# Kernel tuning notes

Measured on AMD Instinct MI355X. Metric: run time of the kernel, lower is better.

## Reference

```python
import jax, jax.numpy as jnp
import numpy as np

DIM = 1024
HEADS = 16
HEAD_DIM = 64
CHUNK = 128
B = 2
S = 2048  # 2 * N * CHUNK with N = 8


def rotate_half(x):
    # interleaved pair rotation: (x1, x2) -> (-x2, x1)
    x1 = x[..., 0::2]
    x2 = x[..., 1::2]
    return jnp.stack((-x2, x1), axis=-1).reshape(x.shape)


def rms_norm(x, w, eps=1e-6):
    v = jnp.mean(jnp.square(x.astype(jnp.float32)), axis=-1, keepdims=True)
    return (x * jax.lax.rsqrt(v + eps)).astype(x.dtype) * w


def build_chunk_mask(seq_len, chunk_size):
    # Replicates ChunkAttnProcessor training mask (right_mask).
    c = jnp.arange(seq_len) // chunk_size
    ci = c[None, :]   # key-chunk index (columns) -- matches torch's unsqueeze(0)
    cj = c[:, None]   # query-chunk index (rows)  -- matches torch's unsqueeze(1)
    N = seq_len // (2 * chunk_size)  # num_cache_blocks
    max_lookback = 5
    rel_j = cj - N
    mask_self = ci == cj
    mask_cache = (rel_j >= 0) & (ci < N) & (ci < rel_j) & (ci >= rel_j - max_lookback)
    return mask_self | mask_cache  # [S, S] bool, row = query, col = key


def setup_inputs() -> dict:
    key = jax.random.key(0)
    ks = jax.random.split(key, 10)
    x = jax.random.normal(ks[0], (B, S, DIM), jnp.float32)
    mask = jnp.ones((B, S), jnp.bool_)
    # rotary frequency table, interleaved pairs: [S, HEAD_DIM]
    pos = jnp.arange(S, dtype=jnp.float32)
    inv = 1.0 / (10000.0 ** (jnp.arange(0, HEAD_DIM, 2, dtype=jnp.float32) / HEAD_DIM))
    freqs = jnp.repeat(pos[:, None] * inv[None, :], 2, axis=-1)
    inner = HEADS * HEAD_DIM
    sc = 0.02
    Wq = jax.random.normal(ks[1], (inner, DIM), jnp.float32) * sc
    bq = jax.random.normal(ks[2], (inner,), jnp.float32) * sc
    Wk = jax.random.normal(ks[3], (inner, DIM), jnp.float32) * sc
    bk = jax.random.normal(ks[4], (inner,), jnp.float32) * sc
    Wv = jax.random.normal(ks[5], (inner, DIM), jnp.float32) * sc
    bv = jax.random.normal(ks[6], (inner,), jnp.float32) * sc
    Wo = jax.random.normal(ks[7], (DIM, inner), jnp.float32) * sc
    bo = jax.random.normal(ks[8], (DIM,), jnp.float32) * sc
    qw = jnp.ones((HEAD_DIM,), jnp.float32)
    kw = jnp.ones((HEAD_DIM,), jnp.float32)
    return {"x": x, "mask": mask, "freqs": freqs, "Wq": Wq, "bq": bq,
            "Wk": Wk, "bk": bk, "Wv": Wv, "bv": bv, "Wo": Wo, "bo": bo,
            "qw": qw, "kw": kw}


def reference(x, mask, freqs, Wq, bq, Wk, bk, Wv, bv, Wo, bo, qw, kw):
    b, n, _ = x.shape
    # QKV projections (torch Linear: x @ W.T + b)
    q = jnp.einsum('bnd,ed->bne', x, Wq) + bq
    k = jnp.einsum('bnd,ed->bne', x, Wk) + bk
    v = jnp.einsum('bnd,ed->bne', x, Wv) + bv
    q = q.reshape(b, n, HEADS, HEAD_DIM).transpose(0, 2, 1, 3)  # [b,h,n,d]
    k = k.reshape(b, n, HEADS, HEAD_DIM).transpose(0, 2, 1, 3)
    v = v.reshape(b, n, HEADS, HEAD_DIM).transpose(0, 2, 1, 3)
    # qk rms-norm over head_dim
    q = rms_norm(q, qw)
    k = rms_norm(k, kw)
    # rotary embedding (xpos_scale = None -> scale 1.0)
    cos = jnp.cos(freqs)
    sin = jnp.sin(freqs)
    q = q * cos + rotate_half(q) * sin
    k = k * cos + rotate_half(k) * sin
    # block-local + cache-lookback mask (training path), combined with pad mask
    block_mask = build_chunk_mask(n, CHUNK)                                  # [S,S]
    pad = (mask[:, None, :] & mask[:, :, None]) | jnp.eye(n, dtype=bool)[None]
    amask = (block_mask[None] & pad)[:, None]                                # [b,1,S,S]
    # masked SDPA
    scale = 1.0 / np.sqrt(HEAD_DIM)
    logits = jnp.einsum('bhqd,bhkd->bhqk', q, k) * scale
    logits = jnp.where(amask, logits, -jnp.inf)
    attn = jax.nn.softmax(logits, axis=-1)
    o = jnp.einsum('bhqk,bhkd->bhqd', attn, v)
    o = o.transpose(0, 2, 1, 3).reshape(b, n, HEADS * HEAD_DIM)
    o = jnp.einsum('bne,de->bnd', o, Wo) + bo
    o = jnp.where(mask[..., None], o, 0.0)
    return o
```

## Files before the change

### kernel.cpp

```cpp
#include <hip/hip_runtime.h>
#include <stdint.h>

typedef unsigned short u16;
typedef __bf16 bf16x8 __attribute__((ext_vector_type(8)));
typedef float f32x4 __attribute__((ext_vector_type(4)));
typedef u16 u16x8 __attribute__((ext_vector_type(8)));

#define DIMD 1024
#define SLEN 2048
#define NHEAD 16
#define HD 64

static __device__ __forceinline__ float b2f(u16 u){ union{float f;uint32_t i;}x; x.i=((uint32_t)u)<<16; return x.f; }
static __device__ __forceinline__ u16 f2b(float f){ union{float f;uint32_t i;}x; x.f=f; uint32_t r=x.i+0x7FFFu+((x.i>>16)&1u); return (u16)(r>>16); }
static __device__ __forceinline__ u16 f2b_fast(float f){ __bf16 h=(__bf16)f; return __builtin_bit_cast(u16,h); }

static __device__ __forceinline__ void gl_lds16(const u16* g, u16* l){
  __builtin_amdgcn_global_load_lds((__attribute__((address_space(1))) void*)g,
                                   (__attribute__((address_space(3))) void*)l, 16, 0, 0);
}
static __device__ __forceinline__ f32x4 mfma16(bf16x8 a, bf16x8 b, f32x4 c){
  return __builtin_amdgcn_mfma_f32_16x16x32_bf16(a, b, c, 0, 0, 0);
}

__global__ __launch_bounds__(256) void k_convert(const float* __restrict__ x,
    const float* __restrict__ wq, const float* __restrict__ wk,
    const float* __restrict__ wv, const float* __restrict__ wo,
    u16* __restrict__ ws)
{
  const int y = blockIdx.y;
  const float* src; u16* dst; int n;
  if (y==0){ src=x;  dst=ws;           n=1<<22; }
  else if (y==1){ src=wq; dst=ws+(4u<<20); n=1<<20; }
  else if (y==2){ src=wk; dst=ws+(5u<<20); n=1<<20; }
  else if (y==3){ src=wv; dst=ws+(6u<<20); n=1<<20; }
  else          { src=wo; dst=ws+(7u<<20); n=1<<20; }
  const int idx = (blockIdx.x*256 + threadIdx.x)*8;
  if (idx >= n) return;
  const float4* s4 = (const float4*)(src+idx);
  float4 a = s4[0], b = s4[1];
  u16x8 r;
  r[0]=f2b(a.x); r[1]=f2b(a.y); r[2]=f2b(a.z); r[3]=f2b(a.w);
  r[4]=f2b(b.x); r[5]=f2b(b.y); r[6]=f2b(b.z); r[7]=f2b(b.w);
  *(u16x8*)(dst+idx) = r;
}

__global__ __launch_bounds__(256,2) void k_gemm_qkv(const u16* __restrict__ A,
    const u16* __restrict__ wq, const u16* __restrict__ wk, const u16* __restrict__ wv,
    const float* __restrict__ bq, const float* __restrict__ bk, const float* __restrict__ bv,
    u16* __restrict__ qo, u16* __restrict__ ko, u16* __restrict__ vo)
{
  __shared__ u16 Al[128*32];
  __shared__ u16 Bl[128*32];
  const int tid = threadIdx.x, lane = tid&63, w = tid>>6;
  const int L15 = lane&15, g = lane>>4;
  const int mb = blockIdx.x;
  const int yy = blockIdx.y;
  const int t = yy>>3, nb = yy&7;
  const u16* Bm = (t==0)?wq:((t==1)?wk:wv);
  const float* bias = (t==0)?bq:((t==1)?bk:bv);
  u16* dst = (t==0)?qo:((t==1)?ko:vo);
  const int wm=(w&1)*64, wn=(w>>1)*64;
  f32x4 acc[4][4];
  #pragma unroll
  for(int i=0;i<4;++i){
    #pragma unroll
    for(int j=0;j<4;++j) acc[i][j]=0;
  }
  const u16* Ab = A  + (size_t)mb*128*DIMD;
  const u16* Bb = Bm + (size_t)nb*128*DIMD;
  const int srow = lane>>2, scol = (lane&3)*8;
  for (int kt=0; kt<32; ++kt){
    const int kk = kt*32;
    #pragma unroll
    for (int c2=0;c2<2;++c2){
      const int c = w*2+c2;
      gl_lds16(Ab + (c*16+srow)*DIMD + kk + scol, Al + c*512);
      gl_lds16(Bb + (c*16+srow)*DIMD + kk + scol, Bl + c*512);
    }
    __syncthreads();
    bf16x8 af[4], bf[4];
    #pragma unroll
    for (int mt=0;mt<4;++mt) af[mt]=*(const bf16x8*)(Al + (wm+mt*16+L15)*32 + g*8);
    #pragma unroll
    for (int nt=0;nt<4;++nt) bf[nt]=*(const bf16x8*)(Bl + (wn+nt*16+L15)*32 + g*8);
    #pragma unroll
    for (int mt=0;mt<4;++mt){
      #pragma unroll
      for (int nt=0;nt<4;++nt)
        acc[mt][nt]=mfma16(af[mt], bf[nt], acc[mt][nt]);
    }
    __syncthreads();
  }
  #pragma unroll
  for (int nt=0;nt<4;++nt){
    const int c = nb*128 + wn + nt*16 + L15;
    const float bv_ = bias[c];
    const int h = c>>6, d = c&63;
    #pragma unroll
    for (int mt=0;mt<4;++mt){
      #pragma unroll
      for (int r=0;r<4;++r){
        const int rowM = mb*128 + wm + mt*16 + g*4 + r;
        const int b_ = rowM>>11, s = rowM&(SLEN-1);
        dst[((size_t)((b_*NHEAD+h)*SLEN+s))*HD + d] = f2b(acc[mt][nt][r]+bv_);
      }
    }
  }
}

__global__ __launch_bounds__(256,2) void k_gemm_out(const u16* __restrict__ A,
    const u16* __restrict__ Bm, const float* __restrict__ bias, float* __restrict__ out)
{
  __shared__ u16 Al[128*32];
  __shared__ u16 Bl[128*32];
  const int tid = threadIdx.x, lane = tid&63, w = tid>>6;
  const int L15 = lane&15, g = lane>>4;
  const int mb = blockIdx.x;
  const int nb = blockIdx.y;
  const int wm=(w&1)*64, wn=(w>>1)*64;
  f32x4 acc[4][4];
  #pragma unroll
  for(int i=0;i<4;++i){
    #pragma unroll
    for(int j=0;j<4;++j) acc[i][j]=0;
  }
  const u16* Ab = A  + (size_t)mb*128*DIMD;
  const u16* Bb = Bm + (size_t)nb*128*DIMD;
  const int srow = lane>>2, scol = (lane&3)*8;
  for (int kt=0; kt<32; ++kt){
    const int kk = kt*32;
    #pragma unroll
    for (int c2=0;c2<2;++c2){
      const int c = w*2+c2;
      gl_lds16(Ab + (c*16+srow)*DIMD + kk + scol, Al + c*512);
      gl_lds16(Bb + (c*16+srow)*DIMD + kk + scol, Bl + c*512);
    }
    __syncthreads();
    bf16x8 af[4], bf[4];
    #pragma unroll
    for (int mt=0;mt<4;++mt) af[mt]=*(const bf16x8*)(Al + (wm+mt*16+L15)*32 + g*8);
    #pragma unroll
    for (int nt=0;nt<4;++nt) bf[nt]=*(const bf16x8*)(Bl + (wn+nt*16+L15)*32 + g*8);
    #pragma unroll
    for (int mt=0;mt<4;++mt){
      #pragma unroll
      for (int nt=0;nt<4;++nt)
        acc[mt][nt]=mfma16(af[mt], bf[nt], acc[mt][nt]);
    }
    __syncthreads();
  }
  #pragma unroll
  for (int nt=0;nt<4;++nt){
    const int c = nb*128 + wn + nt*16 + L15;
    const float bv_ = bias[c];
    #pragma unroll
    for (int mt=0;mt<4;++mt){
      #pragma unroll
      for (int r=0;r<4;++r){
        const int rowM = mb*128 + wm + mt*16 + g*4 + r;
        out[(size_t)rowM*DIMD + c] = acc[mt][nt][r]+bv_;
      }
    }
  }
}

__global__ __launch_bounds__(256) void k_rope(u16* __restrict__ qb, u16* __restrict__ kb,
    const float* __restrict__ freqs, const float* __restrict__ qw, const float* __restrict__ kw)
{
  const int tid=threadIdx.x, lane=tid&63, w=tid>>6;
  const int rid = blockIdx.x*4 + w;
  u16* buf; const float* wt; float scale;
  if (blockIdx.y==0){ buf=qb; wt=qw; scale=0.125f; } else { buf=kb; wt=kw; scale=1.0f; }
  const int s = rid & (SLEN-1);
  const size_t off = (size_t)rid*HD + lane;
  float v = b2f(buf[off]);
  float ss = v*v;
  #pragma unroll
  for (int m=32;m;m>>=1) ss += __shfl_xor(ss, m);
  float xn = v * rsqrtf(ss*(1.0f/HD) + 1e-6f) * wt[lane];
  float fr = freqs[s*HD + lane];
  float cs = __cosf(fr), sn = __sinf(fr);
  float pa = __shfl_xor(xn, 1);
  float rot = (lane&1) ? pa : -pa;
  buf[off] = f2b((xn*cs + rot*sn)*scale);
}

__global__ __launch_bounds__(256,2) void k_attn(const u16* __restrict__ qb, const u16* __restrict__ kb,
    const u16* __restrict__ vb, u16* __restrict__ ob)
{
  __shared__ u16 VT[64*128];
  __shared__ u16 Kl[128*64];
  __shared__ u16 Pl[4*32*128];
  const int tid=threadIdx.x, lane=tid&63, w=tid>>6;
  const int L15=lane&15, g=lane>>4;
  const int bid=blockIdx.x;
  const int qc=bid&15, h=(bid>>4)&15, b_=bid>>8;
  const size_t bh=(size_t)(b_*NHEAD+h);
  const u16* qp = qb + (bh*SLEN + qc*128)*HD;

  bf16x8 qf[2][2];
  #pragma unroll
  for (int mt=0;mt<2;++mt){
    #pragma unroll
    for (int ks=0;ks<2;++ks)
      qf[mt][ks]=*(const bf16x8*)(qp + (w*32+mt*16+L15)*HD + ks*32 + g*8);
  }

  f32x4 accO[2][4];
  float ps[2][4];
  #pragma unroll
  for (int mt=0;mt<2;++mt){
    #pragma unroll
    for(int nt=0;nt<4;++nt) accO[mt][nt]=0;
    #pragma unroll
    for(int r=0;r<4;++r) ps[mt][r]=0.f;
  }

  int kcs[6]; int nk=0; kcs[nk++]=qc;
  if (qc>=9){
    int lo=qc-13; if(lo<0)lo=0;
    const int hi=qc-9;
    for(int kc=lo;kc<=hi;++kc) kcs[nk++]=kc;
  }
  u16* Pw = Pl + w*32*128;

  for (int it=0; it<nk; ++it){
    const int kc=kcs[it];
    const u16* kp = kb + (bh*SLEN + kc*128)*HD;
    const u16* vp = vb + (bh*SLEN + kc*128)*HD;
    #pragma unroll
    for (int i=0;i<4;++i){
      const int idx = i*256 + tid;
      const int row = idx>>3, k8 = idx&7;
      u16x8 kv = *(const u16x8*)(kp + row*HD + k8*8);
      *(u16x8*)(Kl + row*HD + 8*(k8 ^ (row&7))) = kv;
    }
    #pragma unroll
    for (int p=0;p<2;++p){
      const int k0 = p*64 + (tid&31)*2;
      const int dc = (tid>>5)*8;
      u16x8 v0 = *(const u16x8*)(vp + k0*HD + dc);
      u16x8 v1 = *(const u16x8*)(vp + (k0+1)*HD + dc);
      #pragma unroll
      for (int j=0;j<8;++j){
        const int d = dc+j;
        const int kx = k0 ^ ((d&7)<<3);
        *(uint32_t*)(VT + d*128 + kx) = (uint32_t)v0[j] | ((uint32_t)v1[j]<<16);
      }
    }
    __syncthreads();
    #pragma unroll
    for (int mt=0;mt<2;++mt){
      f32x4 sfr[8];
      #pragma unroll
      for (int nt=0;nt<8;++nt){
        const int row = nt*16+L15;
        const u16* kr = Kl + row*HD;
        bf16x8 kf0 = *(const bf16x8*)(kr + 8*((g  ) ^ (row&7)));
        bf16x8 kf1 = *(const bf16x8*)(kr + 8*((g+4) ^ (row&7)));
        f32x4 cc=0;
        cc=mfma16(qf[mt][0],kf0,cc);
        cc=mfma16(qf[mt][1],kf1,cc);
        sfr[nt]=cc;
      }
      #pragma unroll
      for (int nt=0;nt<8;++nt){
        const int col=nt*16+L15;
        #pragma unroll
        for (int r=0;r<4;++r){
          float pv=__expf(sfr[nt][r]);
          ps[mt][r]+=pv;
          const int row=mt*16+g*4+r;
          Pw[row*128 + (col ^ ((row&15)<<3))]=f2b_fast(pv);
        }
      }
    }
    #pragma unroll
    for (int ks=0;ks<4;++ks){
      bf16x8 pf[2], vf[4];
      #pragma unroll
      for (int mt=0;mt<2;++mt){
        const int row=mt*16+L15;
        pf[mt]=*(const bf16x8*)(Pw + row*128 + ((ks*32+g*8) ^ ((row&15)<<3)));
      }
      #pragma unroll
      for (int nt=0;nt<4;++nt){
        const int n=nt*16+L15;
        vf[nt]=*(const bf16x8*)(VT + n*128 + ((ks*32+g*8) ^ ((n&7)<<3)));
      }
      #pragma unroll
      for (int mt=0;mt<2;++mt){
        #pragma unroll
        for (int nt=0;nt<4;++nt)
          accO[mt][nt]=mfma16(pf[mt],vf[nt],accO[mt][nt]);
      }
    }
    __syncthreads();
  }

  #pragma unroll
  for (int mt=0;mt<2;++mt){
    #pragma unroll
    for (int r=0;r<4;++r){
      float l=ps[mt][r];
      #pragma unroll
      for (int sh=1; sh<16; sh<<=1) l+=__shfl_xor(l,sh);
      const float inv=1.0f/l;
      const int srow=qc*128 + w*32 + mt*16 + g*4 + r;
      #pragma unroll
      for (int nt=0;nt<4;++nt){
        const size_t di=((size_t)(b_*SLEN+srow))*DIMD + h*HD + nt*16 + L15;
        ob[di]=f2b_fast(accO[mt][nt][r]*inv);
      }
    }
  }
}

extern "C" void kernel_launch(void* const* d_in, const int* in_sizes, int n_in,
                              void* d_out, int out_size, void* d_ws, size_t ws_size,
                              hipStream_t stream)
{
  (void)in_sizes; (void)n_in; (void)out_size; (void)ws_size;
  const float* x     = (const float*)d_in[0];
  const float* freqs = (const float*)d_in[2];
  const float* Wq    = (const float*)d_in[3];
  const float* bq    = (const float*)d_in[4];
  const float* Wk    = (const float*)d_in[5];
  const float* bk    = (const float*)d_in[6];
  const float* Wv    = (const float*)d_in[7];
  const float* bv    = (const float*)d_in[8];
  const float* Wo    = (const float*)d_in[9];
  const float* bo    = (const float*)d_in[10];
  const float* qw    = (const float*)d_in[11];
  const float* kw    = (const float*)d_in[12];

  u16* ws  = (u16*)d_ws;
  u16* xb  = ws;
  u16* wqb = ws + (4u<<20);
  u16* wkb = ws + (5u<<20);
  u16* wvb = ws + (6u<<20);
  u16* wob = ws + (7u<<20);
  u16* q   = ws + (8u<<20);
  u16* k   = ws + (12u<<20);
  u16* v   = ws + (16u<<20);
  u16* o   = ws + (20u<<20);

  k_convert<<<dim3(2048,5),256,0,stream>>>(x,Wq,Wk,Wv,Wo,ws);
  k_gemm_qkv<<<dim3(32,24),256,0,stream>>>(xb,wqb,wkb,wvb,bq,bk,bv,q,k,v);
  k_rope<<<dim3(16384,2),256,0,stream>>>(q,k,freqs,qw,kw);
  k_attn<<<512,256,0,stream>>>(q,k,v,o);
  k_gemm_out<<<dim3(32,8),256,0,stream>>>(o,wob,bo,(float*)d_out);
}
```

Before: 198.6 us.

## Fuse QK RMS-norm and rotary into QKV GEMM epilogue; reorder attention chunks

The separate rope kernel is removed. RMS-norm, rotary embedding and the q scaling now run in the QKV GEMM epilogue, using cross-lane shuffles over the 16-lane groups that each hold one head's 64 columns. This drops a kernel launch and a full read-modify-write pass over q and k. Separately, the attention block-to-chunk mapping is reversed for batch 1, likely to spread the uneven per-chunk work across the grid. The epilogue gets heavier, with more shuffles and transcendental calls per GEMM tile, which may raise register pressure.

```diff
diff --git a/kernel.cpp b/kernel.cpp
--- a/kernel.cpp
+++ b/kernel.cpp
@@ -48,6 +48,7 @@
 __global__ __launch_bounds__(256,2) void k_gemm_qkv(const u16* __restrict__ A,
     const u16* __restrict__ wq, const u16* __restrict__ wk, const u16* __restrict__ wv,
     const float* __restrict__ bq, const float* __restrict__ bk, const float* __restrict__ bv,
+    const float* __restrict__ freqs, const float* __restrict__ qw, const float* __restrict__ kw,
     u16* __restrict__ qo, u16* __restrict__ ko, u16* __restrict__ vo)
 {
   __shared__ u16 Al[128*32];
@@ -92,18 +93,54 @@
     }
     __syncthreads();
   }
-  #pragma unroll
-  for (int nt=0;nt<4;++nt){
-    const int c = nb*128 + wn + nt*16 + L15;
-    const float bv_ = bias[c];
-    const int h = c>>6, d = c&63;
+  float bias_v[4];
+  #pragma unroll
+  for (int nt=0;nt<4;++nt) bias_v[nt] = bias[nb*128 + wn + nt*16 + L15];
+
+  if (t < 2){
+    const float* wt = (t==0)? qw : kw;
+    const float scale = (t==0)? 0.125f : 1.0f;
+    const int h = (nb*128 + wn) >> 6;
+    float wt_v[4];
+    #pragma unroll
+    for (int nt=0;nt<4;++nt) wt_v[nt] = wt[nt*16 + L15];
     #pragma unroll
     for (int mt=0;mt<4;++mt){
       #pragma unroll
       for (int r=0;r<4;++r){
+        float val[4]; float ss=0.f;
+        #pragma unroll
+        for (int nt=0;nt<4;++nt){ val[nt]=acc[mt][nt][r]+bias_v[nt]; ss+=val[nt]*val[nt]; }
+        #pragma unroll
+        for (int sh=1; sh<16; sh<<=1) ss += __shfl_xor(ss, sh);
+        const float rin = rsqrtf(ss*(1.0f/HD) + 1e-6f);
         const int rowM = mb*128 + wm + mt*16 + g*4 + r;
-        const int b_ = rowM>>11, s = rowM&(SLEN-1);
-        dst[((size_t)((b_*NHEAD+h)*SLEN+s))*HD + d] = f2b(acc[mt][nt][r]+bv_);
+        const int b2 = rowM>>11, s = rowM&(SLEN-1);
+        const size_t rb = ((size_t)((b2*NHEAD+h)*SLEN+s))*HD;
+        #pragma unroll
+        for (int nt=0;nt<4;++nt){
+          const int d = nt*16 + L15;
+          float xn = val[nt]*rin*wt_v[nt];
+          float fr = freqs[s*HD + d];
+          float pa = __shfl_xor(xn, 1);
+          float rot = (L15&1) ? pa : -pa;
+          dst[rb + d] = f2b((xn*__cosf(fr) + rot*__sinf(fr))*scale);
+        }
+      }
+    }
+  } else {
+    #pragma unroll
+    for (int nt=0;nt<4;++nt){
+      const int c = nb*128 + wn + nt*16 + L15;
+      const int h = c>>6, d = c&63;
+      #pragma unroll
+      for (int mt=0;mt<4;++mt){
+        #pragma unroll
+        for (int r=0;r<4;++r){
+          const int rowM = mb*128 + wm + mt*16 + g*4 + r;
+          const int b2 = rowM>>11, s = rowM&(SLEN-1);
+          dst[((size_t)((b2*NHEAD+h)*SLEN+s))*HD + d] = f2b(acc[mt][nt][r]+bias_v[nt]);
+        }
       }
     }
   }
@@ -165,27 +202,6 @@
   }
 }
 
-__global__ __launch_bounds__(256) void k_rope(u16* __restrict__ qb, u16* __restrict__ kb,
-    const float* __restrict__ freqs, const float* __restrict__ qw, const float* __restrict__ kw)
-{
-  const int tid=threadIdx.x, lane=tid&63, w=tid>>6;
-  const int rid = blockIdx.x*4 + w;
-  u16* buf; const float* wt; float scale;
-  if (blockIdx.y==0){ buf=qb; wt=qw; scale=0.125f; } else { buf=kb; wt=kw; scale=1.0f; }
-  const int s = rid & (SLEN-1);
-  const size_t off = (size_t)rid*HD + lane;
-  float v = b2f(buf[off]);
-  float ss = v*v;
-  #pragma unroll
-  for (int m=32;m;m>>=1) ss += __shfl_xor(ss, m);
-  float xn = v * rsqrtf(ss*(1.0f/HD) + 1e-6f) * wt[lane];
-  float fr = freqs[s*HD + lane];
-  float cs = __cosf(fr), sn = __sinf(fr);
-  float pa = __shfl_xor(xn, 1);
-  float rot = (lane&1) ? pa : -pa;
-  buf[off] = f2b((xn*cs + rot*sn)*scale);
-}
-
 __global__ __launch_bounds__(256,2) void k_attn(const u16* __restrict__ qb, const u16* __restrict__ kb,
     const u16* __restrict__ vb, u16* __restrict__ ob)
 {
@@ -195,7 +211,11 @@
   const int tid=threadIdx.x, lane=tid&63, w=tid>>6;
   const int L15=lane&15, g=lane>>4;
   const int bid=blockIdx.x;
-  const int qc=bid&15, h=(bid>>4)&15, b_=bid>>8;
+  const int b_=bid>>8;
+  const int t2=bid&255;
+  const int h=(t2>>4)&15;
+  const int c0=t2&15;
+  const int qc = b_ ? (15-c0) : c0;
   const size_t bh=(size_t)(b_*NHEAD+h);
   const u16* qp = qb + (bh*SLEN + qc*128)*HD;
 
@@ -347,8 +367,7 @@
   u16* o   = ws + (20u<<20);
 
   k_convert<<<dim3(2048,5),256,0,stream>>>(x,Wq,Wk,Wv,Wo,ws);
-  k_gemm_qkv<<<dim3(32,24),256,0,stream>>>(xb,wqb,wkb,wvb,bq,bk,bv,q,k,v);
-  k_rope<<<dim3(16384,2),256,0,stream>>>(q,k,freqs,qw,kw);
+  k_gemm_qkv<<<dim3(32,24),256,0,stream>>>(xb,wqb,wkb,wvb,bq,bk,bv,freqs,qw,kw,q,k,v);
   k_attn<<<512,256,0,stream>>>(q,k,v,o);
   k_gemm_out<<<dim3(32,8),256,0,stream>>>(o,wob,bo,(float*)d_out);
 }
```

New measurement: 179.5 us. 9.6% less time.
